# Kernel optimization log

Hardware: AMD Instinct MI355X
Metric: run time of the kernel (lower is better)

Reference implementation:

```python
import jax, jax.numpy as jnp
import numpy as np

# Constants hardcoded in SpikingNN.__init__
T, DT = 50.0, 0.125
PREF, PMIN, PTH = 0.0, -1.0, 25.0
D, PSPIKE, TREF = 0.25, 4.0, 5.0
TIME = jnp.asarray(np.arange(0, T + DT, DT), dtype=jnp.float32)  # [401]


def setup_inputs() -> dict:
    key = jax.random.key(0)
    k1, k2 = jax.random.split(key)
    N, L = 131072, TIME.shape[0]  # 131072 traces x 401 timesteps
    S = jax.random.uniform(k1, (N, L), dtype=jnp.float32)
    Pn = jax.random.normal(k2, (N, L), dtype=jnp.float32)  # never read before write; shape only
    return {"Pn": Pn, "S": S}


def _forward(S):
    # S: [N, L]; sequential LIF scan over time, vectorized over N traces.
    t0 = TIME[0]
    P0 = S[:, 0] - D                       # i == 0 branch
    spike0 = P0 >= PTH
    P0 = jnp.where(spike0, P0 + PSPIKE, P0)
    t_rest0 = jnp.where(spike0, t0 + TREF, jnp.zeros_like(P0))  # self.t_rest starts at 0

    def step(carry, xs):
        P_prev, t_rest = carry
        s, t = xs
        # refractory: clamp to Pref; else integrate if above Pmin, else reset to 0
        P = jnp.where(t <= t_rest, PREF,
                      jnp.where(P_prev > PMIN, P_prev + s - D, 0.0))
        spike = P >= PTH
        P = jnp.where(spike, P + PSPIKE, P)        # spike overshoot marker
        t_rest = jnp.where(spike, t + TREF, t_rest)  # enter refractory period
        return (P, t_rest), P

    # scan over time axis: xs are ([L-1, N] currents, [L-1] times)
    (_, _), Ps = jax.lax.scan(step, (P0, t_rest0), (S[:, 1:].T, TIME[1:]))
    return jnp.concatenate([P0[:, None], Ps.T], axis=1)  # [N, L]


def reference(Pn, S):
    # Pn is overwritten in-place in the original before any element is read.
    return _forward(S)
```

## Files before the change

### kernel.cpp

```cpp
#include <hip/hip_runtime.h>


#define NT    131072
#define L     401
#define BLKT  256
#define CHUNK 32
#define NCH   13

__global__ __launch_bounds__(BLKT) void snn_scan_kernel(
    const float* __restrict__ S, float* __restrict__ out)
{
    __shared__ float smem[2][BLKT * CHUNK];

    const int tid  = threadIdx.x;
    const int lane = tid & 63;
    const int wave = tid >> 6;
    const int l5   = lane >> 5;
    const int c5   = lane & 31;
    const int tkey = tid & 31;

    const int rowBase = blockIdx.x * BLKT;
    const int wRow    = wave * 64;

    {
        float pre[CHUNK];
        #pragma unroll
        for (int k = 0; k < CHUNK; ++k) {
            const int riw = 2 * k + l5;
            pre[k] = S[(rowBase + wRow + riw) * L + c5];
        }
        #pragma unroll
        for (int k = 0; k < CHUNK; ++k) {
            const int riw = 2 * k + l5;
            smem[0][(wRow + riw) * CHUNK + (c5 ^ (riw & 31))] = pre[k];
        }
    }

    float P = 0.0f, t_rest = -1.0f;

    #pragma unroll 1
    for (int cc = 0; cc < NCH; ++cc) {
        const int c0 = cc * CHUNK;
        float* __restrict__ bcur = smem[cc & 1];
        float* __restrict__ bnxt = smem[(cc + 1) & 1];

        float pre[CHUNK];
        const bool have_next = (cc + 1 < NCH);
        if (have_next) {
            const int c0n = c0 + CHUNK;
            #pragma unroll
            for (int k = 0; k < CHUNK; ++k) {
                const int riw = 2 * k + l5;
                pre[k] = (c0n + c5 < L)
                       ? S[(rowBase + wRow + riw) * L + c0n + c5]
                       : 0.0f;
            }
        }
        asm volatile("" ::: "memory");

        float s[CHUNK];
        #pragma unroll
        for (int j = 0; j < CHUNK; ++j)
            s[j] = bcur[tid * CHUNK + (j ^ tkey)];

        float r[CHUNK];
        #pragma unroll
        for (int j = 0; j < CHUNK; ++j) {
            const float t = (float)(c0 + j) * 0.125f;
            float p = (t <= t_rest)
                    ? 0.0f
                    : ((P > -1.0f) ? (P + s[j]) - 0.25f : 0.0f);
            const bool spike = (p >= 25.0f);
            p      = spike ? p + 4.0f : p;
            t_rest = spike ? t + 5.0f : t_rest;
            r[j] = p;
            P    = p;
        }
        #pragma unroll
        for (int j = 0; j < CHUNK; ++j)
            bcur[tid * CHUNK + (j ^ tkey)] = r[j];

        #pragma unroll
        for (int k = 0; k < CHUNK; ++k) {
            const int riw = 2 * k + l5;
            const float v = bcur[(wRow + riw) * CHUNK + c5];
            const int col = c5 ^ (riw & 31);
            if (c0 + col < L)
                out[(rowBase + wRow + riw) * L + c0 + col] = v;
        }

        asm volatile("" ::: "memory");

        if (have_next) {
            #pragma unroll
            for (int k = 0; k < CHUNK; ++k) {
                const int riw = 2 * k + l5;
                bnxt[(wRow + riw) * CHUNK + (c5 ^ (riw & 31))] = pre[k];
            }
        }
    }
}

extern "C" void kernel_launch(void* const* d_in, const int* in_sizes, int n_in,
                              void* d_out, int out_size, void* d_ws, size_t ws_size,
                              hipStream_t stream)
{
    const float* S   = (const float*)d_in[1];
    float*       out = (float*)d_out;

    snn_scan_kernel<<<NT / BLKT, BLKT, 0, stream>>>(S, out);
}
```

Baseline: 529.2 us.

## Stage input chunks directly into LDS via global_load_lds with per-wave buffers

Replaces the register-staged prefetch (global load into registers, then store to LDS) with __builtin_amdgcn_global_load_lds, which writes global data straight into per-wave double-buffered LDS slices. Each wave now owns its own LDS region, and the pipeline is driven by explicit vmcnt waits instead of register prefetch arrays. The goal is to free the 32 prefetch registers and cut LDS write instructions. The risk is that the hand-written vmcnt counts must line up with the 32 loads per stage and with the output stores that share the counter. Out-of-range columns are clamped to column 400 rather than zero-filled.

```diff
diff --git a/kernel.cpp b/kernel.cpp
--- a/kernel.cpp
+++ b/kernel.cpp
@@ -1,103 +1,88 @@
 #include <hip/hip_runtime.h>
 
 
-#define NT    131072
-#define L     401
-#define BLKT  256
-#define CHUNK 32
-#define NCH   13
+#define L_STEPS 401
+#define NCHUNK  13
+#define CHUNK   32
+#define BLKT    256
+#define SLICE   (64 * CHUNK)
+
+typedef const __attribute__((address_space(1))) void* gas1_t;
+typedef __attribute__((address_space(3))) void*       las3_t;
 
 __global__ __launch_bounds__(BLKT) void snn_scan_kernel(
     const float* __restrict__ S, float* __restrict__ out)
 {
-    __shared__ float smem[2][BLKT * CHUNK];
+    __shared__ float smem[4][2][SLICE];
 
-    const int tid  = threadIdx.x;
-    const int lane = tid & 63;
-    const int wave = tid >> 6;
-    const int l5   = lane >> 5;
-    const int c5   = lane & 31;
-    const int tkey = tid & 31;
-
-    const int rowBase = blockIdx.x * BLKT;
-    const int wRow    = wave * 64;
-
-    {
-        float pre[CHUNK];
-        #pragma unroll
-        for (int k = 0; k < CHUNK; ++k) {
-            const int riw = 2 * k + l5;
-            pre[k] = S[(rowBase + wRow + riw) * L + c5];
-        }
-        #pragma unroll
-        for (int k = 0; k < CHUNK; ++k) {
-            const int riw = 2 * k + l5;
-            smem[0][(wRow + riw) * CHUNK + (c5 ^ (riw & 31))] = pre[k];
-        }
-    }
+    const int tid       = threadIdx.x;
+    const int wave      = tid >> 6;
+    const int lane      = tid & 63;
+    const int traceBase = blockIdx.x * BLKT + wave * 64;
 
     float P = 0.0f, t_rest = -1.0f;
 
+    auto stage = [&](int ccol, int b) {
+        #pragma unroll
+        for (int k = 0; k < 32; ++k) {
+            const int s_  = k * 64 + lane;
+            const int row = s_ >> 5;
+            const int col = (s_ & 31) ^ (row & 31);
+            int gc = ccol + col;
+            if (gc > 400) gc = 400;
+            const float* gp = S + (traceBase + row) * L_STEPS + gc;
+            __builtin_amdgcn_global_load_lds(
+                (gas1_t)gp, (las3_t)&smem[wave][b][k * 64], 4, 0, 0);
+        }
+    };
+
+    stage(0, 0);
+    asm volatile("s_waitcnt vmcnt(0)" ::: "memory");
+
     #pragma unroll 1
-    for (int cc = 0; cc < NCH; ++cc) {
-        const int c0 = cc * CHUNK;
-        float* __restrict__ bcur = smem[cc & 1];
-        float* __restrict__ bnxt = smem[(cc + 1) & 1];
+    for (int c = 0; c < NCHUNK; ++c) {
+        const int c0 = c * CHUNK;
+        const int b  = c & 1;
 
-        float pre[CHUNK];
-        const bool have_next = (cc + 1 < NCH);
-        if (have_next) {
-            const int c0n = c0 + CHUNK;
-            #pragma unroll
-            for (int k = 0; k < CHUNK; ++k) {
-                const int riw = 2 * k + l5;
-                pre[k] = (c0n + c5 < L)
-                       ? S[(rowBase + wRow + riw) * L + c0n + c5]
-                       : 0.0f;
-            }
-        }
+        if (c) asm volatile("s_waitcnt vmcnt(32)" ::: "memory");
+
+        float sv[CHUNK];
+        #pragma unroll
+        for (int j = 0; j < CHUNK; ++j)
+            sv[j] = smem[wave][b][lane * CHUNK + (j ^ (lane & 31))];
         asm volatile("" ::: "memory");
 
-        float s[CHUNK];
-        #pragma unroll
-        for (int j = 0; j < CHUNK; ++j)
-            s[j] = bcur[tid * CHUNK + (j ^ tkey)];
+        if (c + 1 < NCHUNK) stage(c0 + CHUNK, (c + 1) & 1);
+        asm volatile("" ::: "memory");
 
-        float r[CHUNK];
         #pragma unroll
         for (int j = 0; j < CHUNK; ++j) {
             const float t = (float)(c0 + j) * 0.125f;
             float p = (t <= t_rest)
                     ? 0.0f
-                    : ((P > -1.0f) ? (P + s[j]) - 0.25f : 0.0f);
+                    : ((P > -1.0f) ? (P + sv[j]) - 0.25f : 0.0f);
             const bool spike = (p >= 25.0f);
+            t_rest = spike ? t + 5.0f : t_rest;
             p      = spike ? p + 4.0f : p;
-            t_rest = spike ? t + 5.0f : t_rest;
-            r[j] = p;
-            P    = p;
+            sv[j]  = p;
+            P      = p;
         }
+
         #pragma unroll
         for (int j = 0; j < CHUNK; ++j)
-            bcur[tid * CHUNK + (j ^ tkey)] = r[j];
+            smem[wave][b][lane * CHUNK + (j ^ (lane & 31))] = sv[j];
+        asm volatile("" ::: "memory");
 
         #pragma unroll
-        for (int k = 0; k < CHUNK; ++k) {
-            const int riw = 2 * k + l5;
-            const float v = bcur[(wRow + riw) * CHUNK + c5];
-            const int col = c5 ^ (riw & 31);
-            if (c0 + col < L)
-                out[(rowBase + wRow + riw) * L + c0 + col] = v;
+        for (int k = 0; k < 32; ++k) {
+            const int s_  = k * 64 + lane;
+            const int row = s_ >> 5;
+            const int col = (s_ & 31) ^ (row & 31);
+            const int gc  = c0 + col;
+            if (gc < L_STEPS)
+                out[(traceBase + row) * L_STEPS + gc] = smem[wave][b][s_];
         }
-
         asm volatile("" ::: "memory");
-
-        if (have_next) {
-            #pragma unroll
-            for (int k = 0; k < CHUNK; ++k) {
-                const int riw = 2 * k + l5;
-                bnxt[(wRow + riw) * CHUNK + (c5 ^ (riw & 31))] = pre[k];
-            }
-        }
     }
 }
 
@@ -108,5 +93,5 @@
     const float* S   = (const float*)d_in[1];
     float*       out = (float*)d_out;
 
-    snn_scan_kernel<<<NT / BLKT, BLKT, 0, stream>>>(S, out);
+    snn_scan_kernel<<<(131072 / BLKT), BLKT, 0, stream>>>(S, out);
 }
```

Measured after the change: 510.9 us. -3.5%, faster.
